# Kernel tuning notes

Measured on AMD Instinct MI355X. Metric: run time of the kernel, lower is better.

Reference implementation:

```python
import jax, jax.numpy as jnp
import numpy as np


def _rot_grids(group_order, ks, dtype):
    """Normalized sampling grids for each rotation (align_corners=False convention)."""
    k = jnp.arange(group_order, dtype=dtype)
    theta = 2.0 * jnp.pi * k / group_order                      # [G]
    c, s = jnp.cos(theta), jnp.sin(theta)
    # F.affine_grid base coords with align_corners=False: centers of pixels in [-1,1]
    lin = (jnp.arange(ks, dtype=dtype) + 0.5) * (2.0 / ks) - 1.0
    y, x = jnp.meshgrid(lin, lin, indexing='ij')                 # [ks,ks] each
    # theta rows: [cos, -sin, 0], [sin, cos, 0] applied to (x, y, 1)
    gx = c[:, None, None] * x - s[:, None, None] * y             # [G,ks,ks]
    gy = s[:, None, None] * x + c[:, None, None] * y             # [G,ks,ks]
    return gx, gy


def _grid_sample_bilinear_zeros(img, gx, gy):
    """Bilinear grid_sample, padding_mode='zeros', align_corners=False.
    img: [C,H,W]; gx,gy: [G,H,W] normalized coords. Returns [C,G,H,W]."""
    C, H, W = img.shape
    dt = img.dtype
    # unnormalize (align_corners=False)
    ix = ((gx + 1.0) * W - 1.0) * 0.5
    iy = ((gy + 1.0) * H - 1.0) * 0.5
    ix0 = jnp.floor(ix)
    iy0 = jnp.floor(iy)
    wx1 = (ix - ix0).astype(dt); wx0 = 1.0 - wx1
    wy1 = (iy - iy0).astype(dt); wy0 = 1.0 - wy1

    def gather(iyf, ixf):
        xi = ixf.astype(jnp.int32)
        yi = iyf.astype(jnp.int32)
        valid = ((xi >= 0) & (xi < W) & (yi >= 0) & (yi < H)).astype(dt)
        xi_c = jnp.clip(xi, 0, W - 1)
        yi_c = jnp.clip(yi, 0, H - 1)
        return img[:, yi_c, xi_c] * valid                        # [C,G,H,W]

    out = (gather(iy0, ix0) * (wy0 * wx0)
           + gather(iy0, ix0 + 1.0) * (wy0 * wx1)
           + gather(iy0 + 1.0, ix0) * (wy1 * wx0)
           + gather(iy0 + 1.0, ix0 + 1.0) * (wy1 * wx1))
    return out


def setup_inputs() -> dict:
    key = jax.random.key(0)
    out_ch, in_ch, ks = 512, 256, 9
    base_weight = jax.random.normal(key, (out_ch, in_ch, ks, ks), dtype=jnp.float32)
    return {"base_weight": base_weight, "group_order": 8}


def reference(base_weight, group_order):
    O, I, ks, _ = base_weight.shape
    img = base_weight.reshape(O * I, ks, ks)                     # [C,H,W]
    gx, gy = _rot_grids(group_order, ks, base_weight.dtype)      # [G,ks,ks]
    out = _grid_sample_bilinear_zeros(img, gx, gy)               # [C,G,ks,ks]
    # concat over rotations along dim 0 -> [G*O, I, ks, ks]
    out = out.reshape(O, I, group_order, ks, ks).transpose(2, 0, 1, 3, 4)
    return out.reshape(group_order * O, I, ks, ks)
```

## Files before the change

kernel.cpp:

```cpp
#include <hip/hip_runtime.h>


#define KS    9
#define NPIX  81
#define NC    64
#define BLOCK 256
#define NSLOT ((NC * NPIX) / 4)

struct Tap { int qA, qB; float w0, w1, w2, w3; };

constexpr double SQ2H = 0.70710678118654752440084436210485;
constexpr double CS[8] = {1.0,  SQ2H, 0.0, -SQ2H, -1.0, -SQ2H,  0.0,  SQ2H};
constexpr double SN[8] = {0.0,  SQ2H, 1.0,  SQ2H,  0.0, -SQ2H, -1.0, -SQ2H};

constexpr int cfloor(double v) { int i = (int)v; return (v < (double)i) ? i - 1 : i; }

constexpr Tap mk(int g, int p) {
    int py = p / KS, px = p - KS * py;
    double lx = ((double)px + 0.5) * (2.0 / KS) - 1.0;
    double ly = ((double)py + 0.5) * (2.0 / KS) - 1.0;
    double gx = CS[g] * lx - SN[g] * ly;
    double gy = SN[g] * lx + CS[g] * ly;
    double ix = ((gx + 1.0) * KS - 1.0) * 0.5;
    double iy = ((gy + 1.0) * KS - 1.0) * 0.5;
    int x0 = cfloor(ix), y0 = cfloor(iy);
    double fx = ix - x0, fy = iy - y0;
    double wx0 = 1.0 - fx, wx1 = fx;
    double pw0 = 0.0, pw1 = 0.0; int xs = 0;
    if (x0 >= 0 && x0 < KS - 1)      { xs = x0;     pw0 = wx0; pw1 = wx1; }
    else if (x0 == KS - 1)           { xs = KS - 2; pw0 = 0.0; pw1 = wx0; }
    else if (x0 == -1)               { xs = 0;      pw0 = wx1; pw1 = 0.0; }
    int yA = y0, yB = y0 + 1;
    double wyA = (yA >= 0 && yA < KS) ? (1.0 - fy) : 0.0;
    double wyB = (yB >= 0 && yB < KS) ? fy : 0.0;
    int yAc = yA < 0 ? 0 : (yA > KS - 1 ? KS - 1 : yA);
    int yBc = yB < 0 ? 0 : (yB > KS - 1 ? KS - 1 : yB);
    return Tap{ yAc * KS + xs, yBc * KS + xs,
                (float)(wyA * pw0), (float)(wyA * pw1),
                (float)(wyB * pw0), (float)(wyB * pw1) };
}

struct TapTab { Tap t[8][NPIX]; };
constexpr TapTab build_tab() {
    TapTab T{};
    for (int g = 0; g < 8; ++g)
        for (int p = 0; p < NPIX; ++p) T.t[g][p] = mk(g, p);
    return T;
}
constexpr TapTab TT = build_tab();

__device__ __forceinline__ void bar_lds() {
    __builtin_amdgcn_sched_barrier(0);
    asm volatile("s_waitcnt lgkmcnt(0)" ::: "memory");
    __builtin_amdgcn_s_barrier();
    __builtin_amdgcn_sched_barrier(0);
}

template<int G, int P>
__device__ __forceinline__ void one_out(const float (&r)[NPIX], float* otrow) {
    constexpr Tap t = TT.t[G][P];
    float v = 0.0f;
    if constexpr (t.w0 != 0.0f) v += r[t.qA]     * t.w0;
    if constexpr (t.w1 != 0.0f) v += r[t.qA + 1] * t.w1;
    if constexpr (t.w2 != 0.0f) v += r[t.qB]     * t.w2;
    if constexpr (t.w3 != 0.0f) v += r[t.qB + 1] * t.w3;
    otrow[P] = v;
}

template<int G, int P0, int NP>
__device__ __forceinline__ void compute_range(const float (&r)[NPIX], float* otrow) {
    if constexpr (NP > 0) {
        one_out<G, P0>(r, otrow);
        compute_range<G, P0 + 1, NP - 1>(r, otrow);
    }
}

template<int G>
__device__ __forceinline__ void compute_quarter(int gq, const float (&r)[NPIX],
                                                float* otrow) {
    if (gq == 0)      compute_range<G,  0, 20>(r, otrow);
    else if (gq == 1) compute_range<G, 20, 20>(r, otrow);
    else if (gq == 2) compute_range<G, 40, 20>(r, otrow);
    else              compute_range<G, 60, 21>(r, otrow);
}

__device__ __forceinline__ void cp_of(int d, int& c, int& p) {
    c = (d * 6473) >> 19;
    p = d - NPIX * c;
}

template<int G>
__device__ __forceinline__ int qe(int p) {
    if constexpr (G == 0) return p;
    else if constexpr (G == 4) return 80 - p;
    else {
        int py = (p * 57) >> 9;
        int px = p - KS * py;
        if constexpr (G == 2) return KS * px + 8 - py;
        else                  return 72 - KS * px + py;
    }
}

template<int G>
__device__ __forceinline__ void flush_even(const float* lin, float* outg, int t) {
    float4* d4 = (float4*)outg;
    if constexpr (G == 0) {
        const float4* s4 = (const float4*)lin;
        for (int j = t; j < NSLOT; j += BLOCK) d4[j] = s4[j];
    } else {
        for (int j = t; j < NSLOT; j += BLOCK) {
            int d0 = 4 * j;
            float v[4];
#pragma unroll
            for (int k = 0; k < 4; ++k) {
                int c, p; cp_of(d0 + k, c, p);
                v[k] = lin[c * NPIX + qe<G>(p)];
            }
            d4[j] = make_float4(v[0], v[1], v[2], v[3]);
        }
    }
}

__device__ __forceinline__ void flush_ot(const float* ot, float* outg, int t) {
    const float4* s4 = (const float4*)ot;
    float4* d4 = (float4*)outg;
    for (int j = t; j < NSLOT; j += BLOCK) d4[j] = s4[j];
}

__global__ __launch_bounds__(BLOCK) void st_rotate(
        const float* __restrict__ in, float* __restrict__ out, int C) {
    __shared__ __align__(16) float lin[NC * NPIX];
    __shared__ __align__(16) float ota[NC * NPIX];
    __shared__ __align__(16) float otb[NC * NPIX];
    const int t = threadIdx.x;
    const int c0 = blockIdx.x * NC;

    {
        const float4* src = (const float4*)(in + (size_t)c0 * NPIX);
        float4* dst = (float4*)lin;
        for (int j = t; j < NSLOT; j += BLOCK) dst[j] = src[j];
    }
    bar_lds();

    const int c = t & 63, gq = t >> 6;
    float* otrowA = &ota[c * NPIX];
    float* otrowB = &otb[c * NPIX];
    float* const ob = out + (size_t)c0 * NPIX;
    const size_t gstride = (size_t)C * NPIX;

    float r[NPIX];
    {
        const float* myrow = &lin[c * NPIX];
#pragma unroll
        for (int j = 0; j < NPIX; ++j) r[j] = myrow[j];
    }

    flush_even<0>(lin, ob, t);
    compute_quarter<1>(gq, r, otrowA);
    bar_lds();
    flush_ot(ota, ob + 1 * gstride, t);
    flush_even<2>(lin, ob + 2 * gstride, t);
    compute_quarter<3>(gq, r, otrowB);
    bar_lds();
    flush_ot(otb, ob + 3 * gstride, t);
    flush_even<4>(lin, ob + 4 * gstride, t);
    compute_quarter<5>(gq, r, otrowA);
    bar_lds();
    flush_ot(ota, ob + 5 * gstride, t);
    flush_even<6>(lin, ob + 6 * gstride, t);
    compute_quarter<7>(gq, r, otrowB);
    bar_lds();
    flush_ot(otb, ob + 7 * gstride, t);
}

extern "C" void kernel_launch(void* const* d_in, const int* in_sizes, int n_in,
                              void* d_out, int out_size, void* d_ws, size_t ws_size,
                              hipStream_t stream) {
    const float* in = (const float*)d_in[0];
    float* out = (float*)d_out;
    const int C = in_sizes[0] / NPIX;
    st_rotate<<<C / NC, BLOCK, 0, stream>>>(in, out, C);
}
```

Before: 365.7 us.

## Split rotations across grid y dimension and use nontemporal output stores

Instead of one block producing all 8 rotations for its 64 channels, the grid gains a y dimension so each block produces a single rotation. Blocks now use one LDS output buffer instead of two, which allows more blocks per CU and gives eight times as many blocks to spread the write-bound workload. Output stores become nontemporal to reduce cache pollution. The cost is that each input tile is read from global memory eight times instead of once, and each odd-rotation block reloads registers.

```diff
diff --git a/kernel.cpp b/kernel.cpp
--- a/kernel.cpp
+++ b/kernel.cpp
@@ -6,6 +6,8 @@
 #define NC    64
 #define BLOCK 256
 #define NSLOT ((NC * NPIX) / 4)
+
+typedef float f4 __attribute__((ext_vector_type(4)));
 
 struct Tap { int qA, qB; float w0, w1, w2, w3; };
 
@@ -56,6 +58,10 @@
     __builtin_amdgcn_sched_barrier(0);
 }
 
+__device__ __forceinline__ void st_nt(f4* dst, f4 v) {
+    __builtin_nontemporal_store(v, dst);
+}
+
 template<int G, int P>
 __device__ __forceinline__ void one_out(const float (&r)[NPIX], float* otrow) {
     constexpr Tap t = TT.t[G][P];
@@ -102,75 +108,64 @@
 }
 
 template<int G>
-__device__ __forceinline__ void flush_even(const float* lin, float* outg, int t) {
-    float4* d4 = (float4*)outg;
+__device__ __forceinline__ void do_even(const float* lin, f4* d4, int t) {
     if constexpr (G == 0) {
-        const float4* s4 = (const float4*)lin;
-        for (int j = t; j < NSLOT; j += BLOCK) d4[j] = s4[j];
+        const f4* s4 = (const f4*)lin;
+        for (int j = t; j < NSLOT; j += BLOCK) st_nt(&d4[j], s4[j]);
     } else {
         for (int j = t; j < NSLOT; j += BLOCK) {
             int d0 = 4 * j;
-            float v[4];
+            f4 v;
 #pragma unroll
             for (int k = 0; k < 4; ++k) {
                 int c, p; cp_of(d0 + k, c, p);
                 v[k] = lin[c * NPIX + qe<G>(p)];
             }
-            d4[j] = make_float4(v[0], v[1], v[2], v[3]);
+            st_nt(&d4[j], v);
         }
     }
 }
 
-__device__ __forceinline__ void flush_ot(const float* ot, float* outg, int t) {
-    const float4* s4 = (const float4*)ot;
-    float4* d4 = (float4*)outg;
-    for (int j = t; j < NSLOT; j += BLOCK) d4[j] = s4[j];
+template<int G>
+__device__ __forceinline__ void do_odd(const float* lin, float* ot,
+                                       f4* d4, int t) {
+    const int c = t & 63, gq = t >> 6;
+    float r[NPIX];
+    const float* myrow = &lin[c * NPIX];
+#pragma unroll
+    for (int j = 0; j < NPIX; ++j) r[j] = myrow[j];
+    compute_quarter<G>(gq, r, &ot[c * NPIX]);
+    bar_lds();
+    const f4* s4 = (const f4*)ot;
+    for (int j = t; j < NSLOT; j += BLOCK) st_nt(&d4[j], s4[j]);
 }
 
 __global__ __launch_bounds__(BLOCK) void st_rotate(
         const float* __restrict__ in, float* __restrict__ out, int C) {
     __shared__ __align__(16) float lin[NC * NPIX];
-    __shared__ __align__(16) float ota[NC * NPIX];
-    __shared__ __align__(16) float otb[NC * NPIX];
+    __shared__ __align__(16) float ot[NC * NPIX];
     const int t = threadIdx.x;
+    const int g = blockIdx.y;
     const int c0 = blockIdx.x * NC;
 
     {
-        const float4* src = (const float4*)(in + (size_t)c0 * NPIX);
-        float4* dst = (float4*)lin;
+        const f4* src = (const f4*)(in + (size_t)c0 * NPIX);
+        f4* dst = (f4*)lin;
         for (int j = t; j < NSLOT; j += BLOCK) dst[j] = src[j];
     }
     bar_lds();
 
-    const int c = t & 63, gq = t >> 6;
-    float* otrowA = &ota[c * NPIX];
-    float* otrowB = &otb[c * NPIX];
-    float* const ob = out + (size_t)c0 * NPIX;
-    const size_t gstride = (size_t)C * NPIX;
-
-    float r[NPIX];
-    {
-        const float* myrow = &lin[c * NPIX];
-#pragma unroll
-        for (int j = 0; j < NPIX; ++j) r[j] = myrow[j];
+    f4* d4 = (f4*)(out + ((size_t)g * C + c0) * NPIX);
+    switch (g) {
+        case 0: do_even<0>(lin, d4, t); break;
+        case 1: do_odd <1>(lin, ot, d4, t); break;
+        case 2: do_even<2>(lin, d4, t); break;
+        case 3: do_odd <3>(lin, ot, d4, t); break;
+        case 4: do_even<4>(lin, d4, t); break;
+        case 5: do_odd <5>(lin, ot, d4, t); break;
+        case 6: do_even<6>(lin, d4, t); break;
+        default: do_odd<7>(lin, ot, d4, t); break;
     }
-
-    flush_even<0>(lin, ob, t);
-    compute_quarter<1>(gq, r, otrowA);
-    bar_lds();
-    flush_ot(ota, ob + 1 * gstride, t);
-    flush_even<2>(lin, ob + 2 * gstride, t);
-    compute_quarter<3>(gq, r, otrowB);
-    bar_lds();
-    flush_ot(otb, ob + 3 * gstride, t);
-    flush_even<4>(lin, ob + 4 * gstride, t);
-    compute_quarter<5>(gq, r, otrowA);
-    bar_lds();
-    flush_ot(ota, ob + 5 * gstride, t);
-    flush_even<6>(lin, ob + 6 * gstride, t);
-    compute_quarter<7>(gq, r, otrowB);
-    bar_lds();
-    flush_ot(otb, ob + 7 * gstride, t);
 }
 
 extern "C" void kernel_launch(void* const* d_in, const int* in_sizes, int n_in,
@@ -179,5 +174,6 @@
     const float* in = (const float*)d_in[0];
     float* out = (float*)d_out;
     const int C = in_sizes[0] / NPIX;
-    st_rotate<<<C / NC, BLOCK, 0, stream>>>(in, out, C);
+    dim3 grid(C / NC, 8, 1);
+    st_rotate<<<grid, BLOCK, 0, stream>>>(in, out, C);
 }
```

Result: slower. 395.2 us (+8.1%).
